# Kernel optimization log

Measured on AMD Instinct MI355X. Metric: run time of the kernel, lower is better.

Reference implementation:

```python
import jax, jax.numpy as jnp
import numpy as np

B, S, E, HID, NH = 32, 512, 512, 512, 8
HD = E // NH  # head dim
A1, A2 = 1024, 1024  # architecture
EPS = 1e-5


def layer_norm(x, g, b):
    mu = jnp.mean(x, axis=-1, keepdims=True)
    var = jnp.mean(jnp.square(x - mu), axis=-1, keepdims=True)
    return (x - mu) * jax.lax.rsqrt(var + EPS) * g + b


def setup_inputs() -> dict:
    key = jax.random.key(0)
    ks = jax.random.split(key, 16)
    w = lambda k, shp: (jax.random.normal(k, shp, dtype=jnp.float32) * 0.02)
    return {
        'x': jax.random.normal(ks[0], (B, S, E), dtype=jnp.float32),
        'in_proj_w': w(ks[1], (3 * E, E)),
        'in_proj_b': jnp.zeros((3 * E,), jnp.float32),
        'out_proj_w': w(ks[2], (E, E)),
        'out_proj_b': jnp.zeros((E,), jnp.float32),
        'ln_g': jnp.ones((HID,), jnp.float32),
        'ln_b': jnp.zeros((HID,), jnp.float32),
        'w_ih': w(ks[3], (4 * HID, E)),
        'w_hh': w(ks[4], (4 * HID, HID)),
        'b_ih': jnp.zeros((4 * HID,), jnp.float32),
        'b_hh': jnp.zeros((4 * HID,), jnp.float32),
        'fc_w1': w(ks[5], (A1, HID)),
        'fc_b1': jnp.zeros((A1,), jnp.float32),
        'fc_w2': w(ks[6], (A2, A1)),
        'fc_b2': jnp.zeros((A2,), jnp.float32),
        'fc_wo': w(ks[7], (HID, A2)),
        'fc_bo': jnp.zeros((HID,), jnp.float32),
    }


def reference(x, in_proj_w, in_proj_b, out_proj_w, out_proj_b, ln_g, ln_b,
              w_ih, w_hh, b_ih, b_hh, fc_w1, fc_b1, fc_w2, fc_b2, fc_wo, fc_bo):
    # --- MultiheadAttention (self-attention, batch_first) ---
    qkv = x @ in_proj_w.T + in_proj_b            # [B,S,3E]
    q, k, v = jnp.split(qkv, 3, axis=-1)
    q = q.reshape(B, S, NH, HD)
    k = k.reshape(B, S, NH, HD)
    v = v.reshape(B, S, NH, HD)
    scores = jnp.einsum('bqhd,bkhd->bhqk', q, k) / np.float32(np.sqrt(HD))
    attn = jax.nn.softmax(scores, axis=-1)
    ctx = jnp.einsum('bhqk,bkhd->bqhd', attn, v).reshape(B, S, E)
    attn_out = ctx @ out_proj_w.T + out_proj_b
    attn_out = layer_norm(attn_out + x, ln_g, ln_b)  # [B,S,E]

    # --- LSTMCell unrolled over time via scan ---
    def step(carry, xt):
        hn, cn = carry
        gates = xt @ w_ih.T + b_ih + hn @ w_hh.T + b_hh  # [B,4H]
        i, f, g, o = jnp.split(gates, 4, axis=-1)
        i = jax.nn.sigmoid(i); f = jax.nn.sigmoid(f)
        g = jnp.tanh(g);       o = jax.nn.sigmoid(o)
        cn = f * cn + i * g
        hn = o * jnp.tanh(cn)
        return (hn, cn), hn

    h0 = jnp.zeros((B, HID), jnp.float32)
    c0 = jnp.zeros((B, HID), jnp.float32)
    (hn, cn), hs = jax.lax.scan(step, (h0, c0), attn_out.transpose(1, 0, 2))
    hs = hs.transpose(1, 0, 2)                   # [B,S,HID]

    # --- DeepNeuralNetwork MLP (applied pointwise over timesteps) ---
    h1 = jax.nn.relu(hs @ fc_w1.T + fc_b1)
    h2 = jax.nn.relu(h1 @ fc_w2.T + fc_b2)
    out = h2 @ fc_wo.T + fc_bo                   # [B,S,HID]

    out = layer_norm(out + attn_out, ln_g, ln_b)
    return out, (hn, cn)
```

## Files before the change

kernel.cpp:

```cpp
#include <hip/hip_runtime.h>

#define B_ 32
#define S_ 512
#define E_ 512
#define BS_ (B_*S_)

typedef __bf16 bf16x8 __attribute__((ext_vector_type(8)));
typedef float f32x4 __attribute__((ext_vector_type(4)));
typedef unsigned short u16x8 __attribute__((ext_vector_type(8)));

__device__ __forceinline__ unsigned short f2bf(float f){
  unsigned u = __float_as_uint(f);
  u += 0x7fffu + ((u>>16)&1u);
  return (unsigned short)(u>>16);
}
__device__ __forceinline__ float bf2f(unsigned short u){
  return __uint_as_float(((unsigned)u)<<16);
}
__device__ __forceinline__ float sigm(float x){ return 1.f/(1.f+__expf(-x)); }
__device__ __forceinline__ float tanh_f(float x){
  x = fminf(fmaxf(x,-15.f),15.f);
  float t=__expf(2.f*x); return (t-1.f)/(t+1.f);
}
__device__ __forceinline__ void gload_lds16(const void* g, void* l){
  __builtin_amdgcn_global_load_lds((const __attribute__((address_space(1))) unsigned int*)g,
                                   (__attribute__((address_space(3))) unsigned int*)l, 16, 0, 0);
}

__global__ void cast_bf16_k(const float* __restrict__ in, unsigned short* __restrict__ out, int n4){
  int i = blockIdx.x*256 + threadIdx.x;
  if (i < n4){
    const float4 v = *(const float4*)(in + (size_t)i*4);
    ushort4 o; o.x=f2bf(v.x); o.y=f2bf(v.y); o.z=f2bf(v.z); o.w=f2bf(v.w);
    *(ushort4*)(out + (size_t)i*4) = o;
  }
}
__global__ void addb_k(const float* __restrict__ a, const float* __restrict__ b, float* __restrict__ o, int n){
  int i = blockIdx.x*256 + threadIdx.x;
  if (i < n) o[i] = a[i] + b[i];
}
__global__ void sentinel_k(float* __restrict__ o){ o[0] = 1e9f; }

template<int OUTF , bool RELU>
__global__ __launch_bounds__(256) void gemm_bt(const unsigned short* __restrict__ A,
    const unsigned short* __restrict__ Bw, const float* __restrict__ bias,
    void* __restrict__ Cout, int M, int N, int K){
  __shared__ unsigned short As[128*32];
  __shared__ unsigned short Bs[128*32];
  const int tid = threadIdx.x, lane = tid&63, wid = tid>>6;
  const int bm = blockIdx.y, bn = blockIdx.x;
  const int wr = wid>>1, wc = wid&1;
  const int r = lane&15, kq = lane>>4;
  f32x4 acc[4][4] = {};
  const int nkt = K>>5;
  for (int kt=0; kt<nkt; ++kt){
#pragma unroll
    for (int i=0;i<2;++i){
      int cid = i*256 + tid;
      int row = cid>>2, kc = cid&3;
      int gcol = (kt<<5) + kc*8;
      gload_lds16(A  + (size_t)(bm*128+row)*K + gcol, (char*)As + (i*256 + wid*64)*16);
      gload_lds16(Bw + (size_t)(bn*128+row)*K + gcol, (char*)Bs + (i*256 + wid*64)*16);
    }
    __syncthreads();
    bf16x8 af[4], bfr[4];
#pragma unroll
    for (int i=0;i<4;++i){
      af[i]  = *(const bf16x8*)(As + (wr*64 + i*16 + r)*32 + kq*8);
      bfr[i] = *(const bf16x8*)(Bs + (wc*64 + i*16 + r)*32 + kq*8);
    }
#pragma unroll
    for (int i=0;i<4;++i)
#pragma unroll
      for (int j=0;j<4;++j)
        acc[i][j] = __builtin_amdgcn_mfma_f32_16x16x32_bf16(af[i], bfr[j], acc[i][j], 0,0,0);
    __syncthreads();
  }
#pragma unroll
  for (int j=0;j<4;++j){
    int n = bn*128 + wc*64 + j*16 + r;
    float bv = bias[n];
#pragma unroll
    for (int i=0;i<4;++i){
      int m0 = bm*128 + wr*64 + i*16 + kq*4;
#pragma unroll
      for (int jj=0;jj<4;++jj){
        float v = acc[i][j][jj] + bv;
        if (RELU) v = fmaxf(v, 0.f);
        size_t idx = (size_t)(m0+jj)*N + n;
        if (OUTF==0) ((unsigned short*)Cout)[idx] = f2bf(v);
        else         ((float*)Cout)[idx] = v;
      }
    }
  }
}

__global__ __launch_bounds__(256) void attn_k(const unsigned short* __restrict__ qkv,
                                              unsigned short* __restrict__ ctx){
  __shared__ unsigned short Qs[128*64];
  __shared__ unsigned short Ks[128*64];
  __shared__ unsigned short Vt[64*128];
  __shared__ unsigned short Ps[128*128];
  const int tid=threadIdx.x, lane=tid&63, wid=tid>>6;
  const int qt=blockIdx.x, bh=blockIdx.y, b=bh>>3, h=bh&7;
  const int r=lane&15, kq=lane>>4;
  const int q0=qt*128;
#pragma unroll
  for (int i=0;i<4;++i){
    int cid=i*256+tid; int row=cid>>3, dc=cid&7;
    u16x8 v = *(const u16x8*)(qkv + (size_t)(b*S_+q0+row)*1536 + h*64 + dc*8);
    int byte = (row*128 + dc*16) ^ ((row&7)<<4);
    *(u16x8*)((char*)Qs + byte) = v;
  }
  float m_run[2][4], l_run[2][4];
  f32x4 o_acc[2][4] = {};
#pragma unroll
  for (int a=0;a<2;++a)
#pragma unroll
    for (int j=0;j<4;++j){ m_run[a][j]=-1e30f; l_run[a][j]=0.f; }
  for (int kt=0; kt<4; ++kt){
#pragma unroll
    for (int i=0;i<4;++i){
      int cid=i*256+tid; int row=cid>>3, dc=cid&7;
      u16x8 v = *(const u16x8*)(qkv + (size_t)(b*S_+kt*128+row)*1536 + 512 + h*64 + dc*8);
      int byte = (row*128 + dc*16) ^ ((row&7)<<4);
      *(u16x8*)((char*)Ks + byte) = v;
    }
#pragma unroll
    for (int i=0;i<4;++i){
      int cid=i*256+tid; int sv=cid>>3, dc=cid&7;
      u16x8 v = *(const u16x8*)(qkv + (size_t)(b*S_+kt*128+sv)*1536 + 1024 + h*64 + dc*8);
#pragma unroll
      for (int e=0;e<8;++e){
        int d=dc*8+e;
        int byte = (d*256 + sv*2) ^ ((d&7)<<4);
        *(unsigned short*)((char*)Vt + byte) = (unsigned short)v[e];
      }
    }
    __syncthreads();
    f32x4 sa[2][8] = {};
#pragma unroll
    for (int dstep=0; dstep<2; ++dstep){
      int d0 = dstep*32 + kq*8;
      int q1 = wid*32 + r, q2 = wid*32 + 16 + r;
      bf16x8 a0 = *(const bf16x8*)((char*)Qs + ((q1*128 + d0*2) ^ ((q1&7)<<4)));
      bf16x8 a1 = *(const bf16x8*)((char*)Qs + ((q2*128 + d0*2) ^ ((q2&7)<<4)));
#pragma unroll
      for (int fk=0; fk<8; ++fk){
        int kc = fk*16 + r;
        bf16x8 bk = *(const bf16x8*)((char*)Ks + ((kc*128 + d0*2) ^ ((kc&7)<<4)));
        sa[0][fk] = __builtin_amdgcn_mfma_f32_16x16x32_bf16(a0, bk, sa[0][fk],0,0,0);
        sa[1][fk] = __builtin_amdgcn_mfma_f32_16x16x32_bf16(a1, bk, sa[1][fk],0,0,0);
      }
    }
#pragma unroll
    for (int fq=0; fq<2; ++fq){
#pragma unroll
      for (int j=0;j<4;++j){
        float mx = -1e30f;
#pragma unroll
        for (int fk=0;fk<8;++fk) mx = fmaxf(mx, sa[fq][fk][j]);
        mx *= 0.125f;
#pragma unroll
        for (int off=1; off<16; off<<=1) mx = fmaxf(mx, __shfl_xor(mx, off));
        float mn = fmaxf(m_run[fq][j], mx);
        float corr = __expf(m_run[fq][j] - mn);
        float ps = 0.f;
#pragma unroll
        for (int fk=0;fk<8;++fk){
          float p = __expf(sa[fq][fk][j]*0.125f - mn);
          sa[fq][fk][j] = p; ps += p;
        }
#pragma unroll
        for (int off=1; off<16; off<<=1) ps += __shfl_xor(ps, off);
        l_run[fq][j] = l_run[fq][j]*corr + ps;
        m_run[fq][j] = mn;
#pragma unroll
        for (int fd=0; fd<4; ++fd) o_acc[fq][fd][j] *= corr;
      }
    }
#pragma unroll
    for (int fq=0;fq<2;++fq)
#pragma unroll
      for (int fk=0;fk<8;++fk)
#pragma unroll
        for (int j=0;j<4;++j){
          int qr = wid*32 + fq*16 + kq*4 + j;
          int kc = fk*16 + r;
          int byte = (qr*256 + kc*2) ^ ((qr&7)<<4);
          *(unsigned short*)((char*)Ps + byte) = f2bf(sa[fq][fk][j]);
        }
#pragma unroll
    for (int kk=0;kk<4;++kk){
      int k0 = kk*32 + kq*8;
      bf16x8 pa[2];
#pragma unroll
      for (int fq=0;fq<2;++fq){
        int q = wid*32 + fq*16 + r;
        pa[fq] = *(const bf16x8*)((char*)Ps + ((q*256 + k0*2) ^ ((q&7)<<4)));
      }
#pragma unroll
      for (int fd=0; fd<4; ++fd){
        int d = fd*16 + r;
        bf16x8 bv = *(const bf16x8*)((char*)Vt + ((d*256 + k0*2) ^ ((d&7)<<4)));
        o_acc[0][fd] = __builtin_amdgcn_mfma_f32_16x16x32_bf16(pa[0], bv, o_acc[0][fd],0,0,0);
        o_acc[1][fd] = __builtin_amdgcn_mfma_f32_16x16x32_bf16(pa[1], bv, o_acc[1][fd],0,0,0);
      }
    }
    __syncthreads();
  }
#pragma unroll
  for (int fq=0;fq<2;++fq)
#pragma unroll
    for (int fd=0;fd<4;++fd)
#pragma unroll
      for (int j=0;j<4;++j){
        int qr = q0 + wid*32 + fq*16 + kq*4 + j;
        float v = o_acc[fq][fd][j] / l_run[fq][j];
        ctx[(size_t)(b*S_+qr)*512 + h*64 + fd*16 + r] = f2bf(v);
      }
}

template<bool DUAL>
__global__ __launch_bounds__(64) void ln_k(const float* __restrict__ raw, const float* __restrict__ res,
    const float* __restrict__ gam, const float* __restrict__ bet,
    float* __restrict__ outf, unsigned short* __restrict__ outb){
  const int row=blockIdx.x, lane=threadIdx.x;
  const size_t base=(size_t)row*512 + lane*8;
  float v[8];
  {
    float4 a0=*(const float4*)(raw+base), a1=*(const float4*)(raw+base+4);
    float4 b0=*(const float4*)(res+base), b1=*(const float4*)(res+base+4);
    v[0]=a0.x+b0.x; v[1]=a0.y+b0.y; v[2]=a0.z+b0.z; v[3]=a0.w+b0.w;
    v[4]=a1.x+b1.x; v[5]=a1.y+b1.y; v[6]=a1.z+b1.z; v[7]=a1.w+b1.w;
  }
  float s=0.f;
#pragma unroll
  for (int k=0;k<8;++k) s+=v[k];
#pragma unroll
  for (int off=1;off<64;off<<=1) s+=__shfl_xor(s,off);
  float mu=s*(1.f/512.f);
  float q=0.f;
#pragma unroll
  for (int k=0;k<8;++k){ float d=v[k]-mu; q+=d*d; }
#pragma unroll
  for (int off=1;off<64;off<<=1) q+=__shfl_xor(q,off);
  float rs=rsqrtf(q*(1.f/512.f)+1e-5f);
  float gv[8], bv[8];
  *(float4*)gv=*(const float4*)(gam+lane*8); *(float4*)(gv+4)=*(const float4*)(gam+lane*8+4);
  *(float4*)bv=*(const float4*)(bet+lane*8); *(float4*)(bv+4)=*(const float4*)(bet+lane*8+4);
  float y[8];
#pragma unroll
  for (int k=0;k<8;++k) y[k]=(v[k]-mu)*rs*gv[k]+bv[k];
  *(float4*)(outf+base)   = make_float4(y[0],y[1],y[2],y[3]);
  *(float4*)(outf+base+4) = make_float4(y[4],y[5],y[6],y[7]);
  if (DUAL){
    u16x8 ob;
#pragma unroll
    for (int k=0;k<8;++k) ob[k]=f2bf(y[k]);
    *(u16x8*)(outb+base)=ob;
  }
}

__global__ __launch_bounds__(256,1) void lstm_k(const unsigned short* __restrict__ whh,
    const unsigned short* __restrict__ xpart, unsigned short* __restrict__ hs,
    float* __restrict__ hn_out, float* __restrict__ cn_out, unsigned* __restrict__ bar){
  __shared__ unsigned short Wsl[64*512];
  __shared__ unsigned short Hb[32*512];
  const int tid=threadIdx.x, lane=tid&63, wid=tid>>6;
  const int wg = blockIdx.x;
  const int r=lane&15, kq=lane>>4;
  const int c=r, gate=c&3, uo=(wid<<2)+(c>>2), unit=wg*16+uo;
#pragma unroll
  for (int i=0;i<16;++i){
    int ch=i*256+tid; int lc=ch>>6, kc=ch&63;
    int uoo=((lc>>4)<<2)+((lc&15)>>2), gg=lc&3;
    u16x8 v = *(const u16x8*)(whh + (size_t)(gg*512 + wg*16 + uoo)*512 + kc*8);
    int byte=(lc*1024+kc*16)^((lc&7)<<4);
    *(u16x8*)((char*)Wsl+byte)=v;
  }
  float cst[8]={0,0,0,0,0,0,0,0};
  float hlast[8]={0,0,0,0,0,0,0,0};
  __syncthreads();
  for (int t=0;t<512;++t){
    float xp[8];
#pragma unroll
    for (int s=0;s<8;++s){
      int bb=(s>>2)*16 + kq*4 + (s&3);
      xp[s]=bf2f(xpart[(size_t)(bb*512+t)*2048 + gate*512 + unit]);
    }
    if (t==0){
#pragma unroll
      for (int i=0;i<8;++i){
        int ch=i*256+tid; int bb=ch>>6, kc=ch&63;
        int byte=(bb*1024+kc*16)^((bb&7)<<4);
        u16x8 z={0,0,0,0,0,0,0,0};
        *(u16x8*)((char*)Hb+byte)=z;
      }
    } else {
#pragma unroll
      for (int i=0;i<8;++i){
        int ch=i*256+tid; int bb=ch>>6, kc=ch&63;
        const unsigned long long* gp=(const unsigned long long*)(hs+(size_t)(bb*512+(t-1))*512+kc*8);
        unsigned long long lo=__hip_atomic_load(gp,  __ATOMIC_RELAXED,__HIP_MEMORY_SCOPE_AGENT);
        unsigned long long hi=__hip_atomic_load(gp+1,__ATOMIC_RELAXED,__HIP_MEMORY_SCOPE_AGENT);
        int byte=(bb*1024+kc*16)^((bb&7)<<4);
        *(unsigned long long*)((char*)Hb+byte)=lo;
        *(unsigned long long*)((char*)Hb+byte+8)=hi;
      }
    }
    __syncthreads();
    f32x4 acc[2];
    acc[0][0]=xp[0]; acc[0][1]=xp[1]; acc[0][2]=xp[2]; acc[0][3]=xp[3];
    acc[1][0]=xp[4]; acc[1][1]=xp[5]; acc[1][2]=xp[6]; acc[1][3]=xp[7];
#pragma unroll
    for (int ki=0;ki<16;++ki){
      int k0=ki*32+kq*8;
      int b0=r, b1=16+r;
      bf16x8 a0=*(const bf16x8*)((char*)Hb+((b0*1024+k0*2)^((b0&7)<<4)));
      bf16x8 a1=*(const bf16x8*)((char*)Hb+((b1*1024+k0*2)^((b1&7)<<4)));
      int lc=wid*16+c;
      bf16x8 bw=*(const bf16x8*)((char*)Wsl+((lc*1024+k0*2)^((lc&7)<<4)));
      acc[0]=__builtin_amdgcn_mfma_f32_16x16x32_bf16(a0,bw,acc[0],0,0,0);
      acc[1]=__builtin_amdgcn_mfma_f32_16x16x32_bf16(a1,bw,acc[1],0,0,0);
    }
#pragma unroll
    for (int s=0;s<8;++s){
      float v=acc[s>>2][s&3];
      float n1=__shfl_xor(v,1), n2=__shfl_xor(v,2), n3=__shfl_xor(v,3);
      float g_[4];
      g_[gate]=v; g_[gate^1]=n1; g_[gate^2]=n2; g_[gate^3]=n3;
      float ig=sigm(g_[0]), fg=sigm(g_[1]), gg=tanh_f(g_[2]), og=sigm(g_[3]);
      float cn=fg*cst[s]+ig*gg; cst[s]=cn;
      float hn=og*tanh_f(cn); hlast[s]=hn;
      if (gate==0){
        int bb=(s>>2)*16+kq*4+(s&3);
        unsigned hv=(unsigned)f2bf(hn);
        unsigned long long addr=(unsigned long long)(hs+(size_t)(bb*512+t)*512+unit);
        asm volatile("global_store_short %0, %1, off sc0 sc1" :: "v"(addr), "v"(hv) : "memory");
      }
    }
    asm volatile("s_waitcnt vmcnt(0)" ::: "memory");
    __syncthreads();
    if (tid==0){
      __hip_atomic_fetch_add(bar,1u,__ATOMIC_RELEASE,__HIP_MEMORY_SCOPE_AGENT);
      unsigned target=(unsigned)(32*(t+1));
      while (__hip_atomic_load(bar,__ATOMIC_RELAXED,__HIP_MEMORY_SCOPE_AGENT)<target)
        __builtin_amdgcn_s_sleep(2);
    }
    __syncthreads();
  }
  if (gate==0){
#pragma unroll
    for (int s=0;s<8;++s){
      int bb=(s>>2)*16+kq*4+(s&3);
      hn_out[bb*512+unit]=hlast[s];
      cn_out[bb*512+unit]=cst[s];
    }
  }
}

extern "C" void kernel_launch(void* const* d_in, const int* in_sizes, int n_in,
                              void* d_out, int out_size, void* d_ws, size_t ws_size,
                              hipStream_t stream) {
  const float* x          =(const float*)d_in[0];
  const float* in_proj_w  =(const float*)d_in[1];
  const float* in_proj_b  =(const float*)d_in[2];
  const float* out_proj_w =(const float*)d_in[3];
  const float* out_proj_b =(const float*)d_in[4];
  const float* ln_g       =(const float*)d_in[5];
  const float* ln_b       =(const float*)d_in[6];
  const float* w_ih       =(const float*)d_in[7];
  const float* w_hh       =(const float*)d_in[8];
  const float* b_ih       =(const float*)d_in[9];
  const float* b_hh       =(const float*)d_in[10];
  const float* fc_w1      =(const float*)d_in[11];
  const float* fc_b1      =(const float*)d_in[12];
  const float* fc_w2      =(const float*)d_in[13];
  const float* fc_b2      =(const float*)d_in[14];
  const float* fc_wo      =(const float*)d_in[15];
  const float* fc_bo      =(const float*)d_in[16];

  size_t off=0;
  auto A=[&](size_t b)->char*{ char* p=(char*)d_ws+off; off+=(b+255)&~(size_t)255; return p; };
  unsigned short* wqkv =(unsigned short*)A((size_t)1536*512*2);
  unsigned short* wout =(unsigned short*)A((size_t)512*512*2);
  unsigned short* wih  =(unsigned short*)A((size_t)2048*512*2);
  unsigned short* whh  =(unsigned short*)A((size_t)2048*512*2);
  unsigned short* w1   =(unsigned short*)A((size_t)1024*512*2);
  unsigned short* w2   =(unsigned short*)A((size_t)1024*1024*2);
  unsigned short* wo   =(unsigned short*)A((size_t)512*1024*2);
  float*          biasc=(float*)A(2048*4);
  unsigned*       bar  =(unsigned*)A(256);
  char* regA = A((size_t)BS_*512*2);
  char* regB = A((size_t)BS_*2048*2);
  char* regC = A((size_t)BS_*512*4);
  if (off > ws_size){ sentinel_k<<<1,1,0,stream>>>((float*)d_out); return; }

  unsigned short* xb        =(unsigned short*)regA;
  unsigned short* attn_outb =(unsigned short*)regA;
  unsigned short* hs        =(unsigned short*)regA;
  unsigned short* qkvb      =(unsigned short*)regB;
  unsigned short* ctxb      =(unsigned short*)(regB + (size_t)BS_*1536*2);
  unsigned short* xpart     =(unsigned short*)regB;
  unsigned short* h1b       =(unsigned short*)regB;
  unsigned short* h2b       =(unsigned short*)(regB + (size_t)BS_*1024*2);
  float*          attn_out  =(float*)regC;
  float* outp  =(float*)d_out;
  float* attn_raw = outp;
  float* out_raw  = outp;
  float* hn_out=outp + (size_t)BS_*512;
  float* cn_out=hn_out + (size_t)B_*512;

  auto cast=[&](const float* in, unsigned short* out, size_t n){
    int n4=(int)(n/4);
    cast_bf16_k<<<(n4+255)/256,256,0,stream>>>(in,out,n4);
  };
  cast(x, xb, (size_t)BS_*512);
  cast(in_proj_w, wqkv, (size_t)1536*512);
  cast(out_proj_w, wout, (size_t)512*512);
  cast(w_ih, wih, (size_t)2048*512);
  cast(w_hh, whh, (size_t)2048*512);
  cast(fc_w1, w1, (size_t)1024*512);
  cast(fc_w2, w2, (size_t)1024*1024);
  cast(fc_wo, wo, (size_t)512*1024);
  addb_k<<<8,256,0,stream>>>(b_ih,b_hh,biasc,2048);
  hipMemsetAsync(bar,0,256,stream);

  gemm_bt<0,false><<<dim3(12,128),256,0,stream>>>(xb,wqkv,in_proj_b,qkvb,BS_,1536,512);
  attn_k<<<dim3(4,256),256,0,stream>>>(qkvb,ctxb);
  gemm_bt<1,false><<<dim3(4,128),256,0,stream>>>(ctxb,wout,out_proj_b,attn_raw,BS_,512,512);
  ln_k<true><<<BS_,64,0,stream>>>(attn_raw,x,ln_g,ln_b,attn_out,attn_outb);
  gemm_bt<0,false><<<dim3(16,128),256,0,stream>>>(attn_outb,wih,biasc,xpart,BS_,2048,512);
  lstm_k<<<32,256,0,stream>>>(whh,xpart,hs,hn_out,cn_out,bar);
  gemm_bt<0,true><<<dim3(8,128),256,0,stream>>>(hs,w1,fc_b1,h1b,BS_,1024,512);
  gemm_bt<0,true><<<dim3(8,128),256,0,stream>>>(h1b,w2,fc_b2,h2b,BS_,1024,1024);
  gemm_bt<1,false><<<dim3(4,128),256,0,stream>>>(h2b,wo,fc_bo,out_raw,BS_,512,1024);
  ln_k<false><<<BS_,64,0,stream>>>(out_raw,attn_out,ln_g,ln_b,outp,nullptr);
}
```

Before: 4.132 ms.

## Replace LSTM grid barrier with tagged double-buffered hidden-state exchange

Removes the per-timestep global atomic counter barrier in the persistent LSTM kernel. Each block now publishes its hidden values as 32-bit words pairing the bf16 h with a timestep tag into a double-buffered exchange array, and consumers poll until every tag matches. The layer-norm output is also written in time-major order so the per-step xpart reads are contiguous and can be prefetched one step ahead. The risks are the cost of spinning on wide reads and a bounded spin loop that can exit early and silently use stale data.

```diff
diff --git a/kernel.cpp b/kernel.cpp
--- a/kernel.cpp
+++ b/kernel.cpp
@@ -258,19 +258,25 @@
     u16x8 ob;
 #pragma unroll
     for (int k=0;k<8;++k) ob[k]=f2bf(y[k]);
-    *(u16x8*)(outb+base)=ob;
-  }
-}
-
-__global__ __launch_bounds__(256,1) void lstm_k(const unsigned short* __restrict__ whh,
-    const unsigned short* __restrict__ xpart, unsigned short* __restrict__ hs,
-    float* __restrict__ hn_out, float* __restrict__ cn_out, unsigned* __restrict__ bar){
+    int row2 = ((row&511)<<5) | (row>>9);
+    *(u16x8*)(outb + (size_t)row2*512 + lane*8)=ob;
+  }
+}
+
+__global__ __launch_bounds__(256,1) void lstm_tag_k(
+    const unsigned short* __restrict__ whh,
+    const unsigned short* __restrict__ xpart,
+    unsigned short* __restrict__ hs,
+    float* __restrict__ hn_out, float* __restrict__ cn_out,
+    unsigned* __restrict__ hxch)
+{
   __shared__ unsigned short Wsl[64*512];
   __shared__ unsigned short Hb[32*512];
   const int tid=threadIdx.x, lane=tid&63, wid=tid>>6;
-  const int wg = blockIdx.x;
+  const int wg=blockIdx.x;
   const int r=lane&15, kq=lane>>4;
   const int c=r, gate=c&3, uo=(wid<<2)+(c>>2), unit=wg*16+uo;
+  const int colL=wid*16+c;
 #pragma unroll
   for (int i=0;i<16;++i){
     int ch=i*256+tid; int lc=ch>>6, kc=ch&63;
@@ -279,83 +285,128 @@
     int byte=(lc*1024+kc*16)^((lc&7)<<4);
     *(u16x8*)((char*)Wsl+byte)=v;
   }
-  float cst[8]={0,0,0,0,0,0,0,0};
-  float hlast[8]={0,0,0,0,0,0,0,0};
+  {
+    f32x4 z={0.f,0.f,0.f,0.f};
+#pragma unroll
+    for (int i=0;i<8;++i)
+      *(f32x4*)((char*)Hb + (i*256+tid)*16) = z;
+  }
+  const int gb=tid>>3, gc=tid&7;
+  float cst[8]={0,0,0,0,0,0,0,0}, hlast[8]={0,0,0,0,0,0,0,0};
+  float xpc[8];
+#pragma unroll
+  for (int s=0;s<8;++s){
+    int bb=(s>>2)*16 + kq*4 + (s&3);
+    xpc[s]=bf2f(xpart[(size_t)bb*2048 + gate*512 + unit]);
+  }
   __syncthreads();
   for (int t=0;t<512;++t){
-    float xp[8];
-#pragma unroll
-    for (int s=0;s<8;++s){
-      int bb=(s>>2)*16 + kq*4 + (s&3);
-      xp[s]=bf2f(xpart[(size_t)(bb*512+t)*2048 + gate*512 + unit]);
-    }
-    if (t==0){
-#pragma unroll
-      for (int i=0;i<8;++i){
-        int ch=i*256+tid; int bb=ch>>6, kc=ch&63;
-        int byte=(bb*1024+kc*16)^((bb&7)<<4);
-        u16x8 z={0,0,0,0,0,0,0,0};
-        *(u16x8*)((char*)Hb+byte)=z;
-      }
-    } else {
-#pragma unroll
-      for (int i=0;i<8;++i){
-        int ch=i*256+tid; int bb=ch>>6, kc=ch&63;
-        const unsigned long long* gp=(const unsigned long long*)(hs+(size_t)(bb*512+(t-1))*512+kc*8);
-        unsigned long long lo=__hip_atomic_load(gp,  __ATOMIC_RELAXED,__HIP_MEMORY_SCOPE_AGENT);
-        unsigned long long hi=__hip_atomic_load(gp+1,__ATOMIC_RELAXED,__HIP_MEMORY_SCOPE_AGENT);
-        int byte=(bb*1024+kc*16)^((bb&7)<<4);
-        *(unsigned long long*)((char*)Hb+byte)=lo;
-        *(unsigned long long*)((char*)Hb+byte+8)=hi;
-      }
+    if (t){
+      const unsigned* gp = hxch + (size_t)((t-1)&1)*16384 + gb*512 + gc*64;
+      uint4 w0,w1,w2,w3,w4,w5,w6,w7,w8,w9,wa,wb,wc_,wd,we,wf;
+      const unsigned tg=(unsigned)t;
+      int it=0;
+      for(;;){
+        asm volatile(
+          "global_load_dwordx4 %0, %16, off sc0 sc1\n\t"
+          "global_load_dwordx4 %1, %16, off offset:16 sc0 sc1\n\t"
+          "global_load_dwordx4 %2, %16, off offset:32 sc0 sc1\n\t"
+          "global_load_dwordx4 %3, %16, off offset:48 sc0 sc1\n\t"
+          "global_load_dwordx4 %4, %16, off offset:64 sc0 sc1\n\t"
+          "global_load_dwordx4 %5, %16, off offset:80 sc0 sc1\n\t"
+          "global_load_dwordx4 %6, %16, off offset:96 sc0 sc1\n\t"
+          "global_load_dwordx4 %7, %16, off offset:112 sc0 sc1\n\t"
+          "global_load_dwordx4 %8, %16, off offset:128 sc0 sc1\n\t"
+          "global_load_dwordx4 %9, %16, off offset:144 sc0 sc1\n\t"
+          "global_load_dwordx4 %10, %16, off offset:160 sc0 sc1\n\t"
+          "global_load_dwordx4 %11, %16, off offset:176 sc0 sc1\n\t"
+          "global_load_dwordx4 %12, %16, off offset:192 sc0 sc1\n\t"
+          "global_load_dwordx4 %13, %16, off offset:208 sc0 sc1\n\t"
+          "global_load_dwordx4 %14, %16, off offset:224 sc0 sc1\n\t"
+          "global_load_dwordx4 %15, %16, off offset:240 sc0 sc1\n\t"
+          "s_waitcnt vmcnt(0)"
+          : "=&v"(w0),"=&v"(w1),"=&v"(w2),"=&v"(w3),"=&v"(w4),"=&v"(w5),"=&v"(w6),"=&v"(w7),
+            "=&v"(w8),"=&v"(w9),"=&v"(wa),"=&v"(wb),"=&v"(wc_),"=&v"(wd),"=&v"(we),"=&v"(wf)
+          : "v"(gp) : "memory");
+        bool ok =
+          ((w0.x&0xffffu)==tg)&((w0.y&0xffffu)==tg)&((w0.z&0xffffu)==tg)&((w0.w&0xffffu)==tg)&
+          ((w1.x&0xffffu)==tg)&((w1.y&0xffffu)==tg)&((w1.z&0xffffu)==tg)&((w1.w&0xffffu)==tg)&
+          ((w2.x&0xffffu)==tg)&((w2.y&0xffffu)==tg)&((w2.z&0xffffu)==tg)&((w2.w&0xffffu)==tg)&
+          ((w3.x&0xffffu)==tg)&((w3.y&0xffffu)==tg)&((w3.z&0xffffu)==tg)&((w3.w&0xffffu)==tg)&
+          ((w4.x&0xffffu)==tg)&((w4.y&0xffffu)==tg)&((w4.z&0xffffu)==tg)&((w4.w&0xffffu)==tg)&
+          ((w5.x&0xffffu)==tg)&((w5.y&0xffffu)==tg)&((w5.z&0xffffu)==tg)&((w5.w&0xffffu)==tg)&
+          ((w6.x&0xffffu)==tg)&((w6.y&0xffffu)==tg)&((w6.z&0xffffu)==tg)&((w6.w&0xffffu)==tg)&
+          ((w7.x&0xffffu)==tg)&((w7.y&0xffffu)==tg)&((w7.z&0xffffu)==tg)&((w7.w&0xffffu)==tg)&
+          ((w8.x&0xffffu)==tg)&((w8.y&0xffffu)==tg)&((w8.z&0xffffu)==tg)&((w8.w&0xffffu)==tg)&
+          ((w9.x&0xffffu)==tg)&((w9.y&0xffffu)==tg)&((w9.z&0xffffu)==tg)&((w9.w&0xffffu)==tg)&
+          ((wa.x&0xffffu)==tg)&((wa.y&0xffffu)==tg)&((wa.z&0xffffu)==tg)&((wa.w&0xffffu)==tg)&
+          ((wb.x&0xffffu)==tg)&((wb.y&0xffffu)==tg)&((wb.z&0xffffu)==tg)&((wb.w&0xffffu)==tg)&
+          ((wc_.x&0xffffu)==tg)&((wc_.y&0xffffu)==tg)&((wc_.z&0xffffu)==tg)&((wc_.w&0xffffu)==tg)&
+          ((wd.x&0xffffu)==tg)&((wd.y&0xffffu)==tg)&((wd.z&0xffffu)==tg)&((wd.w&0xffffu)==tg)&
+          ((we.x&0xffffu)==tg)&((we.y&0xffffu)==tg)&((we.z&0xffffu)==tg)&((we.w&0xffffu)==tg)&
+          ((wf.x&0xffffu)==tg)&((wf.y&0xffffu)==tg)&((wf.z&0xffffu)==tg)&((wf.w&0xffffu)==tg);
+        if (ok) break;
+        if (++it>65536) break;
+      }
+      const int base = gb*1024 + gc*128;
+      const int swz = (gb&7)<<4;
+#define PACK2(WA,WB,G) { \
+        uint4 p; \
+        p.x=(WA.x>>16)|(WA.y&0xffff0000u); p.y=(WA.z>>16)|(WA.w&0xffff0000u); \
+        p.z=(WB.x>>16)|(WB.y&0xffff0000u); p.w=(WB.z>>16)|(WB.w&0xffff0000u); \
+        *(uint4*)((char*)Hb + ((base + (G)*16)^swz)) = p; }
+      PACK2(w0,w1,0) PACK2(w2,w3,1) PACK2(w4,w5,2) PACK2(w6,w7,3)
+      PACK2(w8,w9,4) PACK2(wa,wb,5) PACK2(wc_,wd,6) PACK2(we,wf,7)
+#undef PACK2
     }
     __syncthreads();
     f32x4 acc[2];
-    acc[0][0]=xp[0]; acc[0][1]=xp[1]; acc[0][2]=xp[2]; acc[0][3]=xp[3];
-    acc[1][0]=xp[4]; acc[1][1]=xp[5]; acc[1][2]=xp[6]; acc[1][3]=xp[7];
+    acc[0][0]=xpc[0]; acc[0][1]=xpc[1]; acc[0][2]=xpc[2]; acc[0][3]=xpc[3];
+    acc[1][0]=xpc[4]; acc[1][1]=xpc[5]; acc[1][2]=xpc[6]; acc[1][3]=xpc[7];
 #pragma unroll
     for (int ki=0;ki<16;++ki){
-      int k0=ki*32+kq*8;
-      int b0=r, b1=16+r;
-      bf16x8 a0=*(const bf16x8*)((char*)Hb+((b0*1024+k0*2)^((b0&7)<<4)));
-      bf16x8 a1=*(const bf16x8*)((char*)Hb+((b1*1024+k0*2)^((b1&7)<<4)));
-      int lc=wid*16+c;
-      bf16x8 bw=*(const bf16x8*)((char*)Wsl+((lc*1024+k0*2)^((lc&7)<<4)));
+      int kb=ki*64+kq*16;
+      bf16x8 a0=*(const bf16x8*)((char*)Hb+((r*1024+kb)^((r&7)<<4)));
+      bf16x8 a1=*(const bf16x8*)((char*)Hb+(((16+r)*1024+kb)^((r&7)<<4)));
+      bf16x8 bw=*(const bf16x8*)((char*)Wsl+((colL*1024+kb)^((colL&7)<<4)));
       acc[0]=__builtin_amdgcn_mfma_f32_16x16x32_bf16(a0,bw,acc[0],0,0,0);
       acc[1]=__builtin_amdgcn_mfma_f32_16x16x32_bf16(a1,bw,acc[1],0,0,0);
     }
+    float xpn[8]={0,0,0,0,0,0,0,0};
+    if (t<511){
+#pragma unroll
+      for (int s=0;s<8;++s){
+        int bb=(s>>2)*16 + kq*4 + (s&3);
+        xpn[s]=bf2f(xpart[(size_t)((t+1)*32+bb)*2048 + gate*512 + unit]);
+      }
+    }
+    unsigned* pb = hxch + (size_t)(t&1)*16384;
 #pragma unroll
     for (int s=0;s<8;++s){
       float v=acc[s>>2][s&3];
       float n1=__shfl_xor(v,1), n2=__shfl_xor(v,2), n3=__shfl_xor(v,3);
-      float g_[4];
-      g_[gate]=v; g_[gate^1]=n1; g_[gate^2]=n2; g_[gate^3]=n3;
-      float ig=sigm(g_[0]), fg=sigm(g_[1]), gg=tanh_f(g_[2]), og=sigm(g_[3]);
-      float cn=fg*cst[s]+ig*gg; cst[s]=cn;
-      float hn=og*tanh_f(cn); hlast[s]=hn;
       if (gate==0){
-        int bb=(s>>2)*16+kq*4+(s&3);
-        unsigned hv=(unsigned)f2bf(hn);
-        unsigned long long addr=(unsigned long long)(hs+(size_t)(bb*512+t)*512+unit);
-        asm volatile("global_store_short %0, %1, off sc0 sc1" :: "v"(addr), "v"(hv) : "memory");
-      }
-    }
-    asm volatile("s_waitcnt vmcnt(0)" ::: "memory");
-    __syncthreads();
-    if (tid==0){
-      __hip_atomic_fetch_add(bar,1u,__ATOMIC_RELEASE,__HIP_MEMORY_SCOPE_AGENT);
-      unsigned target=(unsigned)(32*(t+1));
-      while (__hip_atomic_load(bar,__ATOMIC_RELAXED,__HIP_MEMORY_SCOPE_AGENT)<target)
-        __builtin_amdgcn_s_sleep(2);
-    }
+        int bb=(s>>2)*16 + kq*4 + (s&3);
+        float ig=sigm(v), fg=sigm(n1), gg2=tanh_f(n2), og=sigm(n3);
+        float cn=fg*cst[s]+ig*gg2; cst[s]=cn;
+        float hn=og*tanh_f(cn); hlast[s]=hn;
+        unsigned h16=(unsigned)f2bf(hn);
+        hs[((size_t)bb*512+t)*512 + unit]=(unsigned short)h16;
+        unsigned word=(h16<<16)|(unsigned)(t+1);
+        unsigned long long ad=(unsigned long long)(pb + bb*512 + unit);
+        asm volatile("global_store_dword %0, %1, off sc0 sc1" :: "v"(ad), "v"(word) : "memory");
+      }
+    }
+#pragma unroll
+    for (int s=0;s<8;++s) xpc[s]=xpn[s];
     __syncthreads();
   }
   if (gate==0){
 #pragma unroll
     for (int s=0;s<8;++s){
-      int bb=(s>>2)*16+kq*4+(s&3);
-      hn_out[bb*512+unit]=hlast[s];
-      cn_out[bb*512+unit]=cst[s];
+      int bb=(s>>2)*16 + kq*4 + (s&3);
+      hn_out[(size_t)bb*512+unit]=hlast[s];
+      cn_out[(size_t)bb*512+unit]=cst[s];
     }
   }
 }
@@ -391,7 +442,7 @@
   unsigned short* w2   =(unsigned short*)A((size_t)1024*1024*2);
   unsigned short* wo   =(unsigned short*)A((size_t)512*1024*2);
   float*          biasc=(float*)A(2048*4);
-  unsigned*       bar  =(unsigned*)A(256);
+  unsigned*       hxch =(unsigned*)A((size_t)2*32*512*4);
   char* regA = A((size_t)BS_*512*2);
   char* regB = A((size_t)BS_*2048*2);
   char* regC = A((size_t)BS_*512*4);
@@ -425,14 +476,14 @@
   cast(fc_w2, w2, (size_t)1024*1024);
   cast(fc_wo, wo, (size_t)512*1024);
   addb_k<<<8,256,0,stream>>>(b_ih,b_hh,biasc,2048);
-  hipMemsetAsync(bar,0,256,stream);
+  hipMemsetAsync(hxch,0,(size_t)2*32*512*4,stream);
 
   gemm_bt<0,false><<<dim3(12,128),256,0,stream>>>(xb,wqkv,in_proj_b,qkvb,BS_,1536,512);
   attn_k<<<dim3(4,256),256,0,stream>>>(qkvb,ctxb);
   gemm_bt<1,false><<<dim3(4,128),256,0,stream>>>(ctxb,wout,out_proj_b,attn_raw,BS_,512,512);
   ln_k<true><<<BS_,64,0,stream>>>(attn_raw,x,ln_g,ln_b,attn_out,attn_outb);
   gemm_bt<0,false><<<dim3(16,128),256,0,stream>>>(attn_outb,wih,biasc,xpart,BS_,2048,512);
-  lstm_k<<<32,256,0,stream>>>(whh,xpart,hs,hn_out,cn_out,bar);
+  lstm_tag_k<<<32,256,0,stream>>>(whh,xpart,hs,hn_out,cn_out,hxch);
   gemm_bt<0,true><<<dim3(8,128),256,0,stream>>>(hs,w1,fc_b1,h1b,BS_,1024,512);
   gemm_bt<0,true><<<dim3(8,128),256,0,stream>>>(h1b,w2,fc_b2,h2b,BS_,1024,1024);
   gemm_bt<1,false><<<dim3(4,128),256,0,stream>>>(h2b,wo,fc_bo,out_raw,BS_,512,1024);
```

Measured after the change: 4.225 ms. 1.02x slower.
